# Optimization experiments

Measured on AMD Instinct MI355X. Metric: run time of the kernel, lower is better.

## Reference

```python
import jax, jax.numpy as jnp
import numpy as np
from functools import partial

B, S = 64, 256
DC, DB = 100, 100           # char / bichar embed dims
VC, VB = 10000, 200000      # vocab sizes
D_IN = (DC + DB) * 2        # 400
D_RNN = 200                 # liner output / LSTM input
H = 256                     # LSTM hidden


def setup_inputs() -> dict:
    key = jax.random.key(0)
    ks = jax.random.split(key, 20)
    s = 0.05
    return {
        "char_features": jax.random.randint(ks[0], (B, S), 0, VC),
        "bichar_left": jax.random.randint(ks[1], (B, S), 0, VB),
        "bichar_right": jax.random.randint(ks[2], (B, S), 0, VB),
        "static_char": jax.random.randint(ks[3], (B, S), 0, VC),
        "static_bichar_left": jax.random.randint(ks[4], (B, S), 0, VB),
        "static_bichar_right": jax.random.randint(ks[5], (B, S), 0, VB),
        "char_emb": jax.random.normal(ks[6], (VC, DC), jnp.float32) * s,
        "bichar_emb": jax.random.normal(ks[7], (VB, DB), jnp.float32) * s,
        "static_char_emb": jax.random.normal(ks[8], (VC, DC), jnp.float32) * s,
        "static_bichar_emb": jax.random.normal(ks[9], (VB, DB), jnp.float32) * s,
        "W_lin": jax.random.normal(ks[10], (D_RNN, D_IN), jnp.float32) * s,
        "b_lin": jnp.zeros((D_RNN,), jnp.float32),
        "Wih_l": jax.random.normal(ks[11], (4 * H, D_RNN), jnp.float32) * s,
        "Whh_l": jax.random.normal(ks[12], (4 * H, H), jnp.float32) * s,
        "bih_l": jnp.zeros((4 * H,), jnp.float32),
        "bhh_l": jnp.zeros((4 * H,), jnp.float32),
        "Wih_r": jax.random.normal(ks[13], (4 * H, D_RNN), jnp.float32) * s,
        "Whh_r": jax.random.normal(ks[14], (4 * H, H), jnp.float32) * s,
        "bih_r": jnp.zeros((4 * H,), jnp.float32),
        "bhh_r": jnp.zeros((4 * H,), jnp.float32),
    }


def _lstm_scan(xs, Wih, Whh, bih, bhh, reverse):
    # xs: [S, B, D_RNN] -> hs: [S, B, H], ordered by original time index
    b = bih + bhh

    def step(carry, x):
        h, c = carry
        gates = x @ Wih.T + h @ Whh.T + b           # [B, 4H]
        i, f, g, o = jnp.split(gates, 4, axis=-1)    # torch LSTMCell gate order
        i, f, o = jax.nn.sigmoid(i), jax.nn.sigmoid(f), jax.nn.sigmoid(o)
        g = jnp.tanh(g)
        c = f * c + i * g
        h = o * jnp.tanh(c)
        return (h, c), h

    init = (jnp.zeros((xs.shape[1], H), xs.dtype), jnp.zeros((xs.shape[1], H), xs.dtype))
    _, hs = jax.lax.scan(step, init, xs, reverse=reverse)
    return hs


def reference(char_features, bichar_left, bichar_right, static_char,
              static_bichar_left, static_bichar_right,
              char_emb, bichar_emb, static_char_emb, static_bichar_emb,
              W_lin, b_lin, Wih_l, Whh_l, bih_l, bhh_l,
              Wih_r, Whh_r, bih_r, bhh_r):
    ch = char_emb[char_features]                       # [B,S,DC]
    sch = static_char_emb[static_char]                 # [B,S,DC]
    bl = bichar_emb[bichar_left]                       # [B,S,DB]
    br = bichar_emb[bichar_right]
    sbl = static_bichar_emb[static_bichar_left]
    sbr = static_bichar_emb[static_bichar_right]

    left = jnp.concatenate([ch, sch, bl, sbl], axis=2)   # [B,S,400]
    right = jnp.concatenate([ch, sch, br, sbr], axis=2)

    left_in = jnp.tanh(left @ W_lin.T + b_lin).transpose(1, 0, 2)    # [S,B,D_RNN]
    right_in = jnp.tanh(right @ W_lin.T + b_lin).transpose(1, 0, 2)

    hs_l = _lstm_scan(left_in, Wih_l, Whh_l, bih_l, bhh_l, reverse=False)  # [S,B,H]
    hs_r = _lstm_scan(right_in, Wih_r, Whh_r, bih_r, bhh_r, reverse=True)  # [S,B,H]

    out = jnp.concatenate([hs_l, hs_r], axis=2).transpose(1, 0, 2)  # [B,S,2H]
    return out
```

## Files before the change

### kernel.cpp

```cpp
#include <hip/hip_runtime.h>
#include <math.h>

#define BB 64
#define SS 256
#define D_IN 400
#define D_RNN 200
#define HID 256
#define G4 1024

#define RHALF 92
#define LHALF 36

#define OFF_WTLIN 0
#define OFF_WTIH  (OFF_WTLIN + 400*200)
#define OFF_WHH16 (OFF_WTIH + 2*200*1024)
#define OFF_X     (OFF_WHH16 + 2*1024*256/2)
#define OFF_GX    (OFF_X + 2*64*256*200)

typedef _Float16 half2_t __attribute__((ext_vector_type(2)));

__device__ __forceinline__ half2_t u2h(unsigned u) {
    union { unsigned u; half2_t h; } x; x.u = u; return x.h;
}

__device__ __forceinline__ float dot2acc(unsigned hu, unsigned wu, float acc) {
#if __has_builtin(__builtin_amdgcn_fdot2)
    return __builtin_amdgcn_fdot2(u2h(hu), u2h(wu), acc, false);
#else
    half2_t h = u2h(hu), w = u2h(wu);
    acc = fmaf((float)h.x, (float)w.x, acc);
    acc = fmaf((float)h.y, (float)w.y, acc);
    return acc;
#endif
}

__device__ __forceinline__ float sigm_f(float x) {
    return 1.0f / (1.0f + __expf(-x));
}
__device__ __forceinline__ float tanh_f(float x) {
    return 2.0f / (1.0f + __expf(-2.0f * x)) - 1.0f;
}

__global__ void kt_wlin(const float* __restrict__ W, float* __restrict__ Wt) {
    int id = blockIdx.x * 256 + threadIdx.x;
    if (id >= D_RNN * D_IN) return;
    int j = id / D_IN, k = id % D_IN;
    Wt[k * D_RNN + j] = W[id];
}

__global__ void kt_wih(const float* __restrict__ Wl, const float* __restrict__ Wr,
                       float* __restrict__ Wt) {
    int id = blockIdx.x * 256 + threadIdx.x;
    if (id >= 2 * G4 * D_RNN) return;
    int dir = id / (G4 * D_RNN);
    int r = id % (G4 * D_RNN);
    int j = r / D_RNN, k = r % D_RNN;
    const float* src = dir ? Wr : Wl;
    Wt[dir * (D_RNN * G4) + k * G4 + j] = src[r];
}

__global__ void kt_whh16(const float* __restrict__ Wl, const float* __restrict__ Wr,
                         _Float16* __restrict__ Wh) {
    int id = blockIdx.x * 256 + threadIdx.x;
    if (id >= 2 * G4 * HID) return;
    int dir = id / (G4 * HID);
    int r = id % (G4 * HID);
    const float* src = dir ? Wr : Wl;
    Wh[dir * (G4 * HID) + r] = (_Float16)src[r];
}

__launch_bounds__(512)
__global__ void k_embed_linear(const int* __restrict__ ci, const int* __restrict__ bli,
                               const int* __restrict__ bri, const int* __restrict__ sci,
                               const int* __restrict__ sbli, const int* __restrict__ sbri,
                               const float* __restrict__ ce, const float* __restrict__ be,
                               const float* __restrict__ sce, const float* __restrict__ sbe,
                               const float* __restrict__ Wt, const float* __restrict__ blin,
                               float* __restrict__ xout) {
    __shared__ __align__(16) float vec[16][2][D_IN];
    __shared__ int idx[16][6];
    int tid = threadIdx.x;
    int g0 = blockIdx.x * 16;

    if (tid < 96) {
        int tt = tid / 6, w = tid % 6;
        int g = g0 + tt;
        const int* arr = (w == 0) ? ci : (w == 1) ? sci : (w == 2) ? bli
                         : (w == 3) ? bri : (w == 4) ? sbli : sbri;
        idx[tt][w] = arr[g];
    }
    __syncthreads();

    for (int v = tid; v < 16 * D_IN; v += 512) {
        int tt = v / D_IN, p = v % D_IN;
        float lv, rv;
        if (p < 100)      { float e = ce[idx[tt][0] * 100 + p];          lv = rv = e; }
        else if (p < 200) { float e = sce[idx[tt][1] * 100 + (p - 100)]; lv = rv = e; }
        else if (p < 300) { int q = p - 200;
                            lv = be[idx[tt][2] * 100 + q];
                            rv = be[idx[tt][3] * 100 + q]; }
        else              { int q = p - 300;
                            lv = sbe[idx[tt][4] * 100 + q];
                            rv = sbe[idx[tt][5] * 100 + q]; }
        vec[tt][0][p] = lv;
        vec[tt][1][p] = rv;
    }
    __syncthreads();

    if (tid < 400) {
        int side = tid / 200, j = tid % 200;
        float acc[16];
        #pragma unroll
        for (int t = 0; t < 16; t++) acc[t] = 0.0f;

        for (int k4 = 0; k4 < D_IN / 4; k4++) {
            float w0 = Wt[(4 * k4 + 0) * D_RNN + j];
            float w1 = Wt[(4 * k4 + 1) * D_RNN + j];
            float w2 = Wt[(4 * k4 + 2) * D_RNN + j];
            float w3 = Wt[(4 * k4 + 3) * D_RNN + j];
            #pragma unroll
            for (int t = 0; t < 16; t++) {
                float4 xv = *(const float4*)&vec[t][side][4 * k4];
                acc[t] += xv.x * w0 + xv.y * w1 + xv.z * w2 + xv.w * w3;
            }
        }
        float bias = blin[j];
        #pragma unroll
        for (int t = 0; t < 16; t++) {
            int g = g0 + t;
            int b = g >> 8, s = g & 255;
            xout[((side * BB + b) * SS + s) * D_RNN + j] = tanh_f(acc[t] + bias);
        }
    }
}

__launch_bounds__(512)
__global__ void k_gatex(const float* __restrict__ x, const float* __restrict__ WtIh,
                        const float* __restrict__ bihl, const float* __restrict__ bhhl,
                        const float* __restrict__ bihr, const float* __restrict__ bhhr,
                        float* __restrict__ gx) {
    __shared__ __align__(16) float xT[D_RNN][36];
    int tid = threadIdx.x;
    int id = blockIdx.x;
    int dir = id >> 9;
    int rem = id & 511;
    int b = rem >> 3;
    int s0 = (rem & 7) * 32;

    const float* xbase = x + ((dir * BB + b) * SS + s0) * D_RNN;
    for (int v = tid; v < 32 * D_RNN; v += 512) {
        int tt = v / D_RNN, k = v % D_RNN;
        xT[k][tt] = xbase[tt * D_RNN + k];
    }
    __syncthreads();

    const float* Wp = WtIh + dir * (D_RNN * G4);
    int j0 = tid, j1 = tid + 512;
    float acc0[32], acc1[32];
    #pragma unroll
    for (int t = 0; t < 32; t++) { acc0[t] = 0.0f; acc1[t] = 0.0f; }

    for (int k = 0; k < D_RNN; k++) {
        float w0 = Wp[k * G4 + j0];
        float w1 = Wp[k * G4 + j1];
        #pragma unroll
        for (int m = 0; m < 8; m++) {
            float4 xv = *(const float4*)&xT[k][4 * m];
            acc0[4 * m + 0] += xv.x * w0;
            acc0[4 * m + 1] += xv.y * w0;
            acc0[4 * m + 2] += xv.z * w0;
            acc0[4 * m + 3] += xv.w * w0;
            acc1[4 * m + 0] += xv.x * w1;
            acc1[4 * m + 1] += xv.y * w1;
            acc1[4 * m + 2] += xv.z * w1;
            acc1[4 * m + 3] += xv.w * w1;
        }
    }

    float bs0, bs1;
    if (dir) { bs0 = bihr[j0] + bhhr[j0]; bs1 = bihr[j1] + bhhr[j1]; }
    else     { bs0 = bihl[j0] + bhhl[j0]; bs1 = bihl[j1] + bhhl[j1]; }

    float* gbase = gx + ((dir * BB + b) * SS + s0) * G4;
    #pragma unroll
    for (int t = 0; t < 32; t++) {
        gbase[t * G4 + j0] = acc0[t] + bs0;
        gbase[t * G4 + j1] = acc1[t] + bs1;
    }
}

__launch_bounds__(1024)
__global__ void k_lstm(const _Float16* __restrict__ whh16, const float* __restrict__ gx,
                       float* __restrict__ out) {
    __shared__ __align__(16) unsigned wlds[9][1024][4];
    __shared__ float gl[G4];
    __shared__ __align__(16) unsigned short hbuf[HID];

    int t = threadIdx.x;
    int bid = blockIdx.x;
    int dir = bid >> 6, b = bid & 63;

    const uint4* wrow = reinterpret_cast<const uint4*>(whh16 + (size_t)(dir * G4 + t) * HID);
    unsigned wr[RHALF];
    #pragma unroll
    for (int i = 0; i < 23; i++) {
        uint4 v = wrow[i];
        wr[4 * i + 0] = v.x; wr[4 * i + 1] = v.y;
        wr[4 * i + 2] = v.z; wr[4 * i + 3] = v.w;
    }
    #pragma unroll
    for (int i = 0; i < 9; i++) {
        uint4 v = wrow[23 + i];
        *reinterpret_cast<uint4*>(&wlds[i][t][0]) = v;
    }

    const float* gxp = gx + (size_t)(dir * BB + b) * SS * G4;
    float* outp = out + (size_t)b * SS * (2 * HID) + dir * HID + t;

    if (t < HID) hbuf[t] = 0;
    float cst = 0.0f;
    __syncthreads();

    int ts = dir ? (SS - 1) : 0;
    int dstep = dir ? -1 : 1;
    float gxv = gxp[(size_t)ts * G4 + t];
    int q = t >> 8;

    const uint4* h4 = reinterpret_cast<const uint4*>(hbuf);

    for (int s = 0; s < SS; s++) {
        float gxn = 0.0f;
        if (s < SS - 1) gxn = gxp[(size_t)(ts + dstep) * G4 + t];

        float a0 = gxv, a1 = 0.0f, a2 = 0.0f, a3 = 0.0f;
        #pragma unroll
        for (int i = 0; i < 23; i++) {
            uint4 hh = h4[i];
            a0 = dot2acc(hh.x, wr[4 * i + 0], a0);
            a1 = dot2acc(hh.y, wr[4 * i + 1], a1);
            a2 = dot2acc(hh.z, wr[4 * i + 2], a2);
            a3 = dot2acc(hh.w, wr[4 * i + 3], a3);
        }
        #pragma unroll
        for (int i = 0; i < 9; i++) {
            uint4 wv = *reinterpret_cast<const uint4*>(&wlds[i][t][0]);
            uint4 hh = h4[23 + i];
            a0 = dot2acc(hh.x, wv.x, a0);
            a1 = dot2acc(hh.y, wv.y, a1);
            a2 = dot2acc(hh.z, wv.z, a2);
            a3 = dot2acc(hh.w, wv.w, a3);
        }
        float gate = (a0 + a1) + (a2 + a3);

        gl[t] = (q == 2) ? tanh_f(gate) : sigm_f(gate);
        __syncthreads();

        if (t < HID) {
            float ig = gl[t];
            float fg = gl[t + 256];
            float gg = gl[t + 512];
            float og = gl[t + 768];
            cst = fg * cst + ig * gg;
            float hh = og * tanh_f(cst);
            outp[(size_t)ts * (2 * HID)] = hh;
            hbuf[t] = __builtin_bit_cast(unsigned short, (_Float16)hh);
        }
        __syncthreads();

        gxv = gxn;
        ts += dstep;
    }
}

extern "C" void kernel_launch(void* const* d_in, const int* in_sizes, int n_in,
                              void* d_out, int out_size, void* d_ws, size_t ws_size,
                              hipStream_t stream) {
    const int* char_features      = (const int*)d_in[0];
    const int* bichar_left        = (const int*)d_in[1];
    const int* bichar_right       = (const int*)d_in[2];
    const int* static_char        = (const int*)d_in[3];
    const int* static_bichar_left = (const int*)d_in[4];
    const int* static_bichar_right= (const int*)d_in[5];
    const float* char_emb         = (const float*)d_in[6];
    const float* bichar_emb       = (const float*)d_in[7];
    const float* static_char_emb  = (const float*)d_in[8];
    const float* static_bichar_emb= (const float*)d_in[9];
    const float* W_lin            = (const float*)d_in[10];
    const float* b_lin            = (const float*)d_in[11];
    const float* Wih_l            = (const float*)d_in[12];
    const float* Whh_l            = (const float*)d_in[13];
    const float* bih_l            = (const float*)d_in[14];
    const float* bhh_l            = (const float*)d_in[15];
    const float* Wih_r            = (const float*)d_in[16];
    const float* Whh_r            = (const float*)d_in[17];
    const float* bih_r            = (const float*)d_in[18];
    const float* bhh_r            = (const float*)d_in[19];

    float* ws    = (float*)d_ws;
    float* wtlin = ws + OFF_WTLIN;
    float* wtih  = ws + OFF_WTIH;
    _Float16* whh16 = (_Float16*)(ws + OFF_WHH16);
    float* xbuf  = ws + OFF_X;
    float* gxbuf = ws + OFF_GX;
    float* out   = (float*)d_out;

    kt_wlin<<<(D_RNN * D_IN + 255) / 256, 256, 0, stream>>>(W_lin, wtlin);
    kt_wih<<<(2 * G4 * D_RNN + 255) / 256, 256, 0, stream>>>(Wih_l, Wih_r, wtih);
    kt_whh16<<<(2 * G4 * HID + 255) / 256, 256, 0, stream>>>(Whh_l, Whh_r, whh16);

    k_embed_linear<<<(BB * SS) / 16, 512, 0, stream>>>(
        char_features, bichar_left, bichar_right, static_char,
        static_bichar_left, static_bichar_right,
        char_emb, bichar_emb, static_char_emb, static_bichar_emb,
        wtlin, b_lin, xbuf);

    k_gatex<<<(2 * BB * SS) / 32, 512, 0, stream>>>(
        xbuf, wtih, bih_l, bhh_l, bih_r, bhh_r, gxbuf);

    k_lstm<<<2 * BB, 1024, 0, stream>>>(whh16, gxbuf, out);
}
```

Measured before the change: 825.9 us.

## Compute all four gates per thread in LSTM kernel, one barrier per step

The recurrent LSTM kernel now uses 256 threads per block, and each thread computes all four gates for one hidden unit. The old version used 1024 threads, one gate each, and exchanged gates through shared memory. Whh is repacked into an interleaved fp16 layout so each thread holds 26 of 32 k-chunks for its four gate rows in registers, with the rest in LDS. The hidden state is double-buffered, which leaves a single __syncthreads per timestep. This removes one barrier and the gate shared-memory round trip per step, in exchange for heavy register pressure (about 416 VGPRs of weights at one wave per EU) and four times more serial dot work per thread.

```diff
diff --git a/kernel.cpp b/kernel.cpp
--- a/kernel.cpp
+++ b/kernel.cpp
@@ -8,13 +8,13 @@
 #define HID 256
 #define G4 1024
 
-#define RHALF 92
-#define LHALF 36
+#define NWREG 26
+#define NWLDS 6
 
 #define OFF_WTLIN 0
 #define OFF_WTIH  (OFF_WTLIN + 400*200)
-#define OFF_WHH16 (OFF_WTIH + 2*200*1024)
-#define OFF_X     (OFF_WHH16 + 2*1024*256/2)
+#define OFF_WPACK (OFF_WTIH + 2*200*1024)
+#define OFF_X     (OFF_WPACK + 2*1024*256/2)
 #define OFF_GX    (OFF_X + 2*64*256*200)
 
 typedef _Float16 half2_t __attribute__((ext_vector_type(2)));
@@ -59,14 +59,15 @@
     Wt[dir * (D_RNN * G4) + k * G4 + j] = src[r];
 }
 
-__global__ void kt_whh16(const float* __restrict__ Wl, const float* __restrict__ Wr,
-                         _Float16* __restrict__ Wh) {
+__global__ void kt_wpack(const float* __restrict__ Wl, const float* __restrict__ Wr,
+                         _Float16* __restrict__ Wp) {
     int id = blockIdx.x * 256 + threadIdx.x;
     if (id >= 2 * G4 * HID) return;
     int dir = id / (G4 * HID);
-    int r = id % (G4 * HID);
+    int rem = id % (G4 * HID);
+    int r = rem / HID, k = rem % HID;
     const float* src = dir ? Wr : Wl;
-    Wh[dir * (G4 * HID) + r] = (_Float16)src[r];
+    Wp[(((size_t)dir * 32 + (k >> 3)) * G4 + r) * 8 + (k & 7)] = (_Float16)src[rem];
 }
 
 __launch_bounds__(512)
@@ -189,85 +190,95 @@
     }
 }
 
-__launch_bounds__(1024)
-__global__ void k_lstm(const _Float16* __restrict__ whh16, const float* __restrict__ gx,
-                       float* __restrict__ out) {
-    __shared__ __align__(16) unsigned wlds[9][1024][4];
-    __shared__ float gl[G4];
-    __shared__ __align__(16) unsigned short hbuf[HID];
+__global__ void
+__attribute__((amdgpu_flat_work_group_size(256, 256), amdgpu_waves_per_eu(1, 1)))
+k_lstm(const _Float16* __restrict__ wpack, const float* __restrict__ gx,
+       float* __restrict__ out) {
+    __shared__ __align__(16) uint4 wlds[4 * NWLDS][256];
+    __shared__ __align__(16) _Float16 hbuf[2][HID];
 
     int t = threadIdx.x;
     int bid = blockIdx.x;
     int dir = bid >> 6, b = bid & 63;
 
-    const uint4* wrow = reinterpret_cast<const uint4*>(whh16 + (size_t)(dir * G4 + t) * HID);
-    unsigned wr[RHALF];
+    const uint4* wp = reinterpret_cast<const uint4*>(wpack) + (size_t)dir * 32 * G4;
+    uint4 w0[NWREG], w1[NWREG], w2[NWREG], w3[NWREG];
     #pragma unroll
-    for (int i = 0; i < 23; i++) {
-        uint4 v = wrow[i];
-        wr[4 * i + 0] = v.x; wr[4 * i + 1] = v.y;
-        wr[4 * i + 2] = v.z; wr[4 * i + 3] = v.w;
+    for (int i = 0; i < NWREG; i++) {
+        w0[i] = wp[i * G4 + 0 * 256 + t];
+        w1[i] = wp[i * G4 + 1 * 256 + t];
+        w2[i] = wp[i * G4 + 2 * 256 + t];
+        w3[i] = wp[i * G4 + 3 * 256 + t];
     }
     #pragma unroll
-    for (int i = 0; i < 9; i++) {
-        uint4 v = wrow[23 + i];
-        *reinterpret_cast<uint4*>(&wlds[i][t][0]) = v;
+    for (int j = 0; j < NWLDS; j++) {
+        wlds[0 * NWLDS + j][t] = wp[(NWREG + j) * G4 + 0 * 256 + t];
+        wlds[1 * NWLDS + j][t] = wp[(NWREG + j) * G4 + 1 * 256 + t];
+        wlds[2 * NWLDS + j][t] = wp[(NWREG + j) * G4 + 2 * 256 + t];
+        wlds[3 * NWLDS + j][t] = wp[(NWREG + j) * G4 + 3 * 256 + t];
     }
 
     const float* gxp = gx + (size_t)(dir * BB + b) * SS * G4;
     float* outp = out + (size_t)b * SS * (2 * HID) + dir * HID + t;
 
-    if (t < HID) hbuf[t] = 0;
+    hbuf[0][t] = (_Float16)0.0f;
     float cst = 0.0f;
     __syncthreads();
 
     int ts = dir ? (SS - 1) : 0;
     int dstep = dir ? -1 : 1;
-    float gxv = gxp[(size_t)ts * G4 + t];
-    int q = t >> 8;
-
-    const uint4* h4 = reinterpret_cast<const uint4*>(hbuf);
+    const float* gcur = gxp + (size_t)ts * G4;
+    float g0 = gcur[t], g1 = gcur[t + 256], g2 = gcur[t + 512], g3 = gcur[t + 768];
 
     for (int s = 0; s < SS; s++) {
-        float gxn = 0.0f;
-        if (s < SS - 1) gxn = gxp[(size_t)(ts + dstep) * G4 + t];
-
-        float a0 = gxv, a1 = 0.0f, a2 = 0.0f, a3 = 0.0f;
-        #pragma unroll
-        for (int i = 0; i < 23; i++) {
+        float n0 = 0.f, n1 = 0.f, n2 = 0.f, n3 = 0.f;
+        if (s < SS - 1) {
+            const float* gn = gxp + (size_t)(ts + dstep) * G4;
+            n0 = gn[t]; n1 = gn[t + 256]; n2 = gn[t + 512]; n3 = gn[t + 768];
+        }
+
+        const uint4* h4 = reinterpret_cast<const uint4*>(hbuf[s & 1]);
+        float a0 = g0, a1 = g1, a2 = g2, a3 = g3;
+        #pragma unroll
+        for (int i = 0; i < NWREG; i++) {
             uint4 hh = h4[i];
-            a0 = dot2acc(hh.x, wr[4 * i + 0], a0);
-            a1 = dot2acc(hh.y, wr[4 * i + 1], a1);
-            a2 = dot2acc(hh.z, wr[4 * i + 2], a2);
-            a3 = dot2acc(hh.w, wr[4 * i + 3], a3);
-        }
-        #pragma unroll
-        for (int i = 0; i < 9; i++) {
-            uint4 wv = *reinterpret_cast<const uint4*>(&wlds[i][t][0]);
-            uint4 hh = h4[23 + i];
-            a0 = dot2acc(hh.x, wv.x, a0);
-            a1 = dot2acc(hh.y, wv.y, a1);
-            a2 = dot2acc(hh.z, wv.z, a2);
-            a3 = dot2acc(hh.w, wv.w, a3);
-        }
-        float gate = (a0 + a1) + (a2 + a3);
-
-        gl[t] = (q == 2) ? tanh_f(gate) : sigm_f(gate);
+            a0 = dot2acc(hh.x, w0[i].x, a0); a0 = dot2acc(hh.y, w0[i].y, a0);
+            a0 = dot2acc(hh.z, w0[i].z, a0); a0 = dot2acc(hh.w, w0[i].w, a0);
+            a1 = dot2acc(hh.x, w1[i].x, a1); a1 = dot2acc(hh.y, w1[i].y, a1);
+            a1 = dot2acc(hh.z, w1[i].z, a1); a1 = dot2acc(hh.w, w1[i].w, a1);
+            a2 = dot2acc(hh.x, w2[i].x, a2); a2 = dot2acc(hh.y, w2[i].y, a2);
+            a2 = dot2acc(hh.z, w2[i].z, a2); a2 = dot2acc(hh.w, w2[i].w, a2);
+            a3 = dot2acc(hh.x, w3[i].x, a3); a3 = dot2acc(hh.y, w3[i].y, a3);
+            a3 = dot2acc(hh.z, w3[i].z, a3); a3 = dot2acc(hh.w, w3[i].w, a3);
+        }
+        #pragma unroll
+        for (int j = 0; j < NWLDS; j++) {
+            uint4 hh = h4[NWREG + j];
+            uint4 v0 = wlds[0 * NWLDS + j][t];
+            uint4 v1 = wlds[1 * NWLDS + j][t];
+            uint4 v2 = wlds[2 * NWLDS + j][t];
+            uint4 v3 = wlds[3 * NWLDS + j][t];
+            a0 = dot2acc(hh.x, v0.x, a0); a0 = dot2acc(hh.y, v0.y, a0);
+            a0 = dot2acc(hh.z, v0.z, a0); a0 = dot2acc(hh.w, v0.w, a0);
+            a1 = dot2acc(hh.x, v1.x, a1); a1 = dot2acc(hh.y, v1.y, a1);
+            a1 = dot2acc(hh.z, v1.z, a1); a1 = dot2acc(hh.w, v1.w, a1);
+            a2 = dot2acc(hh.x, v2.x, a2); a2 = dot2acc(hh.y, v2.y, a2);
+            a2 = dot2acc(hh.z, v2.z, a2); a2 = dot2acc(hh.w, v2.w, a2);
+            a3 = dot2acc(hh.x, v3.x, a3); a3 = dot2acc(hh.y, v3.y, a3);
+            a3 = dot2acc(hh.z, v3.z, a3); a3 = dot2acc(hh.w, v3.w, a3);
+        }
+
+        float ig = sigm_f(a0);
+        float fg = sigm_f(a1);
+        float gg = tanh_f(a2);
+        float og = sigm_f(a3);
+        cst = fg * cst + ig * gg;
+        float hv = og * tanh_f(cst);
+        outp[(size_t)ts * (2 * HID)] = hv;
+        hbuf[(s + 1) & 1][t] = (_Float16)hv;
         __syncthreads();
 
-        if (t < HID) {
-            float ig = gl[t];
-            float fg = gl[t + 256];
-            float gg = gl[t + 512];
-            float og = gl[t + 768];
-            cst = fg * cst + ig * gg;
-            float hh = og * tanh_f(cst);
-            outp[(size_t)ts * (2 * HID)] = hh;
-            hbuf[t] = __builtin_bit_cast(unsigned short, (_Float16)hh);
-        }
-        __syncthreads();
-
-        gxv = gxn;
+        g0 = n0; g1 = n1; g2 = n2; g3 = n3;
         ts += dstep;
     }
 }
@@ -299,14 +310,14 @@
     float* ws    = (float*)d_ws;
     float* wtlin = ws + OFF_WTLIN;
     float* wtih  = ws + OFF_WTIH;
-    _Float16* whh16 = (_Float16*)(ws + OFF_WHH16);
+    _Float16* wpack = (_Float16*)(ws + OFF_WPACK);
     float* xbuf  = ws + OFF_X;
     float* gxbuf = ws + OFF_GX;
     float* out   = (float*)d_out;
 
     kt_wlin<<<(D_RNN * D_IN + 255) / 256, 256, 0, stream>>>(W_lin, wtlin);
     kt_wih<<<(2 * G4 * D_RNN + 255) / 256, 256, 0, stream>>>(Wih_l, Wih_r, wtih);
-    kt_whh16<<<(2 * G4 * HID + 255) / 256, 256, 0, stream>>>(Whh_l, Whh_r, whh16);
+    kt_wpack<<<(2 * G4 * HID + 255) / 256, 256, 0, stream>>>(Whh_l, Whh_r, wpack);
 
     k_embed_linear<<<(BB * SS) / 16, 512, 0, stream>>>(
         char_features, bichar_left, bichar_right, static_char,
@@ -317,5 +328,5 @@
     k_gatex<<<(2 * BB * SS) / 32, 512, 0, stream>>>(
         xbuf, wtih, bih_l, bhh_l, bih_r, bhh_r, gxbuf);
 
-    k_lstm<<<2 * BB, 1024, 0, stream>>>(whh16, gxbuf, out);
-}
+    k_lstm<<<2 * BB, 256, 0, stream>>>(wpack, gxbuf, out);
+}
```

New measurement: 1.061 ms. +28.5%, slower.
